# Optimization experiments

Measured on AMD Instinct MI355X. Metric: run time of the kernel, lower is better.

The kernel has to match this reference:

```python
import jax, jax.numpy as jnp
import numpy as np

QPS = 4           # qubits per split
N_SPLITS = 4
N_LAYERS = 4
NUM_CLASSES = 5
DIM = 16          # 2**QPS statevector dim per split
B = 32768

# PauliZ sign table: zsign[q, idx] = +1 if bit of wire q (wire 0 = MSB) is 0 else -1
_ZSIGN = jnp.asarray(
    1 - 2 * (((np.arange(DIM)[None, :] >> (QPS - 1 - np.arange(QPS)[:, None])) & 1)),
    dtype=jnp.float32)  # [QPS, DIM]


def setup_inputs() -> dict:
    key = jax.random.key(0)
    ks = jax.random.split(key, 8)
    return {
        "x": jax.random.normal(ks[0], (B, N_SPLITS * DIM), jnp.float32),
        "split_weights": jax.random.normal(ks[1], (N_SPLITS, N_LAYERS, QPS, 3), jnp.float32) * 0.1,
        "W1": jax.random.normal(ks[2], (N_SPLITS * QPS, 128), jnp.float32) * 0.1,
        "b1": jnp.zeros((128,), jnp.float32),
        "W2": jax.random.normal(ks[3], (128, 64), jnp.float32) * 0.1,
        "b2": jnp.zeros((64,), jnp.float32),
        "W3": jax.random.normal(ks[4], (64, NUM_CLASSES), jnp.float32) * 0.1,
        "b3": jnp.zeros((NUM_CLASSES,), jnp.float32),
    }


def _apply_1q(state, U, wire):
    """Apply per-split 2x2 unitary U [S,2,2] on `wire` of state [B,S,2,2,2,2]."""
    ax = 2 + wire
    st = jnp.moveaxis(state, ax, -1)
    st = jnp.einsum('sij,bs...j->bs...i', U, st)
    return jnp.moveaxis(st, -1, ax)


def _cnot(state, ctrl, tgt):
    c, t = 2 + ctrl, 2 + tgt
    s0 = jnp.take(state, 0, axis=c)
    s1 = jnp.take(state, 1, axis=c)
    s1 = jnp.flip(s1, axis=t - 1 if t > c else t)
    return jnp.stack([s0, s1], axis=c)


def _quantum_features(x, split_weights):
    b = x.shape[0]
    amps = x.reshape(b, N_SPLITS, DIM)
    # _split_data_symmetrically L2-normalizes each chunk (norm>0 guard)
    norm = jnp.linalg.norm(amps, axis=-1, keepdims=True)
    amps = jnp.where(norm > 0, amps / jnp.where(norm > 0, norm, 1.0), amps)
    state = amps.astype(jnp.complex64).reshape((b, N_SPLITS) + (2,) * QPS)
    for layer in range(N_LAYERS):
        for j in range(QPS):
            hx = split_weights[:, layer, j, 0] * 0.5  # [S]
            hy = split_weights[:, layer, j, 1] * 0.5
            hz = split_weights[:, layer, j, 2] * 0.5
            cx, sx = jnp.cos(hx), jnp.sin(hx)
            cy, sy = jnp.cos(hy), jnp.sin(hy)
            RX = jnp.stack([jnp.stack([cx + 0j, -1j * sx], -1),
                            jnp.stack([-1j * sx, cx + 0j], -1)], -2)
            RY = jnp.stack([jnp.stack([cy + 0j, -sy + 0j], -1),
                            jnp.stack([sy + 0j, cy + 0j], -1)], -2)
            ez = jnp.exp(-1j * hz)
            zero = jnp.zeros_like(ez)
            RZ = jnp.stack([jnp.stack([ez, zero], -1),
                            jnp.stack([zero, jnp.conj(ez)], -1)], -2)
            # applied order RX then RY then RZ => U = RZ @ RY @ RX
            U = jnp.einsum('sij,sjk,skl->sil', RZ, RY, RX)
            state = _apply_1q(state, U, j)
        for j in range(QPS):
            state = _cnot(state, j, (j + 1) % QPS)
    probs = (state.real ** 2 + state.imag ** 2).reshape(b, N_SPLITS, DIM)
    exps = jnp.einsum('bsd,qd->bsq', probs, _ZSIGN)  # <PauliZ_q> per split
    return exps.reshape(b, N_SPLITS * QPS)


def reference(x, split_weights, W1, b1, W2, b2, W3, b3):
    feats = _quantum_features(x, split_weights)
    # aggregation MLP (Dropout is identity in eval mode)
    h = jax.nn.relu(feats @ W1 + b1)
    h = jax.nn.relu(h @ W2 + b2)
    return h @ W3 + b3
```

## Files before the change

kernel.cpp:

```cpp
#include <hip/hip_runtime.h>

#define NSPLIT  4
#define NLAYERS 4
#define QPS     4
#define DIM     16
#define NCLS    5
#define BLK     256
#define RROWS   32

#define U_SS      520
#define FE_STRIDE 17
#define H1_STRIDE 33
#define H2_STRIDE 68

struct c32 { float x, y; };
__device__ __forceinline__ c32 cmul(c32 a, c32 b) { return c32{a.x*b.x - a.y*b.y, a.x*b.y + a.y*b.x}; }
__device__ __forceinline__ c32 cadd(c32 a, c32 b) { return c32{a.x + b.x, a.y + b.y}; }

__global__ void build_unitary_kernel(const float* __restrict__ w,
                                     float* __restrict__ Ur,
                                     float* __restrict__ Ui)
{
    __shared__ float gU[NSPLIT][NLAYERS * QPS][8];

    const int t = threadIdx.x;

    {
        const int s = t >> 4, g = t & 15;
        const float* wp = w + (s * (NLAYERS * QPS) + g) * 3;
        const float hx = 0.5f * wp[0], hy = 0.5f * wp[1], hz = 0.5f * wp[2];
        float sx, cx, sy, cy, sz, cz;
        __sincosf(hx, &sx, &cx);
        __sincosf(hy, &sy, &cy);
        __sincosf(hz, &sz, &cz);
        const c32 X00{cx, 0.f}, X01{0.f, -sx}, X11{cx, 0.f};
        const c32 Y00{cy, 0.f}, Y01{-sy, 0.f}, Y10{sy, 0.f}, Y11{cy, 0.f};
        const c32 Z00{cz, -sz}, Z11{cz, sz};
        const c32 M00 = cadd(cmul(Y00, X00), cmul(Y01, X01));
        const c32 M01 = cadd(cmul(Y00, X01), cmul(Y01, X11));
        const c32 M10 = cadd(cmul(Y10, X00), cmul(Y11, X01));
        const c32 M11 = cadd(cmul(Y10, X01), cmul(Y11, X11));
        const c32 U00 = cmul(Z00, M00), U01 = cmul(Z00, M01);
        const c32 U10 = cmul(Z11, M10), U11 = cmul(Z11, M11);
        float* gp = gU[s][g];
        gp[0] = U00.x; gp[1] = U00.y; gp[2] = U01.x; gp[3] = U01.y;
        gp[4] = U10.x; gp[5] = U10.y; gp[6] = U11.x; gp[7] = U11.y;
    }
    __syncthreads();

    const int s = t >> 4, col = t & 15;
    float str[DIM], sti[DIM];
    #pragma unroll
    for (int d = 0; d < DIM; ++d) { str[d] = (d == col) ? 1.0f : 0.0f; sti[d] = 0.0f; }

    #pragma unroll
    for (int l = 0; l < NLAYERS; ++l) {
        #pragma unroll
        for (int j = 0; j < QPS; ++j) {
            const float* gp = gU[s][l * QPS + j];
            const float4 u0 = *(const float4*)gp;
            const float4 u1 = *(const float4*)(gp + 4);
            const int p = 8 >> j;
            #pragma unroll
            for (int i0 = 0; i0 < DIM; ++i0) {
                if (i0 & p) continue;
                const int i1 = i0 | p;
                const float ar = str[i0], ai = sti[i0];
                const float br = str[i1], bi = sti[i1];
                str[i0] = u0.x*ar - u0.y*ai + u0.z*br - u0.w*bi;
                sti[i0] = u0.x*ai + u0.y*ar + u0.z*bi + u0.w*br;
                str[i1] = u1.x*ar - u1.y*ai + u1.z*br - u1.w*bi;
                sti[i1] = u1.x*ai + u1.y*ar + u1.z*bi + u1.w*br;
            }
        }
        #pragma unroll
        for (int j = 0; j < QPS; ++j) {
            const int pc = 8 >> j, pt = 8 >> ((j + 1) & 3);
            #pragma unroll
            for (int i = 0; i < DIM; ++i) {
                if ((i & pc) && !(i & pt)) {
                    const int i1 = i | pt;
                    float tr = str[i]; str[i] = str[i1]; str[i1] = tr;
                    float ti = sti[i]; sti[i] = sti[i1]; sti[i1] = ti;
                }
            }
        }
    }

    #pragma unroll
    for (int d = 0; d < DIM; ++d) {
        Ur[(s * DIM + d) * DIM + col] = str[d];
        Ui[(s * DIM + d) * DIM + col] = sti[d];
    }
}

__global__ __launch_bounds__(BLK) void qcnn_main_kernel(
    const float* __restrict__ x,
    const float* __restrict__ Ug,
    const float* __restrict__ W1, const float* __restrict__ b1,
    const float* __restrict__ W2, const float* __restrict__ b2,
    const float* __restrict__ W3, const float* __restrict__ b3,
    float* __restrict__ out, int B)
{
    __shared__ __align__(16) float sU[NSPLIT * U_SS];
    __shared__ __align__(16) float sW1[128 * 16];
    __shared__ __align__(16) float sW2[128 * 64];
    __shared__ __align__(16) float sFe[RROWS * FE_STRIDE];
    __shared__ __align__(16) float sH1[128 * H1_STRIDE];
    __shared__ __align__(16) float sH2[RROWS * H2_STRIDE];
    __shared__ float sb1[128], sb2[64], sW3b[64 * NCLS], sb3[NCLS];

    const int t = threadIdx.x;
    const int row0 = blockIdx.x * RROWS;

    {
        const float* Urg = Ug;
        const float* Uig = Ug + 1024;
        for (int i = t; i < 1024; i += BLK) {
            const int s = i >> 8, d = (i >> 4) & 15, c = i & 15;
            const int wd = s * U_SS + d * 32 + 2 * c;
            sU[wd] = Urg[i]; sU[wd + 1] = Uig[i];
        }
        for (int i = t; i < 2048; i += BLK) {
            const int k1 = i >> 4, f = i & 15;
            sW1[i] = W1[f * 128 + k1];
        }
        for (int i = t; i < 2048; i += BLK)
            ((float4*)sW2)[i] = ((const float4*)W2)[i];
        if (t < 128) sb1[t] = b1[t];
        if (t < 64)  sb2[t] = b2[t];
        for (int i = t; i < 64 * NCLS; i += BLK) sW3b[i] = W3[i];
        if (t < NCLS) sb3[t] = b3[t];
    }
    __syncthreads();

    {
        const int u = t >> 1, dh = t & 1;
        const int r = u >> 2, s = u & 3;
        int row = row0 + r; if (row >= B) row = B - 1;

        float v[16];
        const float4* xp = (const float4*)(x + (size_t)row * 64 + s * 16);
        const float4 a0 = xp[0], a1 = xp[1], a2 = xp[2], a3 = xp[3];
        v[0]=a0.x;  v[1]=a0.y;  v[2]=a0.z;  v[3]=a0.w;
        v[4]=a1.x;  v[5]=a1.y;  v[6]=a1.z;  v[7]=a1.w;
        v[8]=a2.x;  v[9]=a2.y;  v[10]=a2.z; v[11]=a2.w;
        v[12]=a3.x; v[13]=a3.y; v[14]=a3.z; v[15]=a3.w;

        float n2 = 0.f;
        #pragma unroll
        for (int c = 0; c < 16; ++c) n2 += v[c] * v[c];
        const float inv2 = (n2 > 0.f) ? (1.0f / n2) : 1.0f;

        float e0 = 0.f, e1 = 0.f, e2 = 0.f, e3 = 0.f;
        const float* ub = sU + s * U_SS + dh * (8 * 32);
        #pragma unroll
        for (int i = 0; i < 8; ++i) {
            const int d = dh * 8 + i;
            const float4* up = (const float4*)(ub + i * 32);
            float yr = 0.f, yi = 0.f;
            #pragma unroll
            for (int cp = 0; cp < 8; ++cp) {
                const float4 uu = up[cp];
                yr += uu.x * v[2*cp] + uu.z * v[2*cp + 1];
                yi += uu.y * v[2*cp] + uu.w * v[2*cp + 1];
            }
            const float p = (yr * yr + yi * yi) * inv2;
            e0 += (d & 8) ? -p : p;
            e1 += (d & 4) ? -p : p;
            e2 += (d & 2) ? -p : p;
            e3 += (d & 1) ? -p : p;
        }
        e0 += __shfl_xor(e0, 1);
        e1 += __shfl_xor(e1, 1);
        e2 += __shfl_xor(e2, 1);
        e3 += __shfl_xor(e3, 1);
        if (dh == 0) {
            float* fp = sFe + r * FE_STRIDE + s * 4;
            fp[0] = e0; fp[1] = e1; fp[2] = e2; fp[3] = e3;
        }
    }
    __syncthreads();

    {
        const int r = t & 31, k1g = t >> 5;
        float fv[16];
        #pragma unroll
        for (int f = 0; f < 16; ++f) fv[f] = sFe[r * FE_STRIDE + f];
        #pragma unroll
        for (int kk = 0; kk < 16; ++kk) {
            const int k1 = k1g * 16 + kk;
            const float4* wp = (const float4*)(sW1 + k1 * 16);
            const float4 w0 = wp[0], w1 = wp[1], w2 = wp[2], w3 = wp[3];
            float a = sb1[k1]
                + w0.x*fv[0]  + w0.y*fv[1]  + w0.z*fv[2]  + w0.w*fv[3]
                + w1.x*fv[4]  + w1.y*fv[5]  + w1.z*fv[6]  + w1.w*fv[7]
                + w2.x*fv[8]  + w2.y*fv[9]  + w2.z*fv[10] + w2.w*fv[11]
                + w3.x*fv[12] + w3.y*fv[13] + w3.z*fv[14] + w3.w*fv[15];
            sH1[k1 * H1_STRIDE + r] = fmaxf(a, 0.f);
        }
    }
    __syncthreads();

    {
        const int oct = t & 7, r = t >> 3;
        float acc[8];
        #pragma unroll
        for (int j = 0; j < 8; ++j) acc[j] = sb2[oct * 8 + j];
        const float*  h1p = sH1 + r;
        const float4* w2p = ((const float4*)sW2) + oct * 2;
        #pragma unroll 4
        for (int k1 = 0; k1 < 128; ++k1) {
            const float h = h1p[k1 * H1_STRIDE];
            const float4 wa = w2p[k1 * 16];
            const float4 wb = w2p[k1 * 16 + 1];
            acc[0] += h * wa.x; acc[1] += h * wa.y; acc[2] += h * wa.z; acc[3] += h * wa.w;
            acc[4] += h * wb.x; acc[5] += h * wb.y; acc[6] += h * wb.z; acc[7] += h * wb.w;
        }
        float4 o0, o1;
        o0.x = fmaxf(acc[0], 0.f); o0.y = fmaxf(acc[1], 0.f);
        o0.z = fmaxf(acc[2], 0.f); o0.w = fmaxf(acc[3], 0.f);
        o1.x = fmaxf(acc[4], 0.f); o1.y = fmaxf(acc[5], 0.f);
        o1.z = fmaxf(acc[6], 0.f); o1.w = fmaxf(acc[7], 0.f);
        float4* hp = (float4*)(sH2 + r * H2_STRIDE + oct * 8);
        hp[0] = o0; hp[1] = o1;
    }
    __syncthreads();

    if (t < RROWS * NCLS) {
        const int r = t / NCLS, j = t - r * NCLS;
        float acc = sb3[j];
        const float4* hp = (const float4*)(sH2 + r * H2_STRIDE);
        #pragma unroll
        for (int q = 0; q < 16; ++q) {
            const float4 h = hp[q];
            acc += h.x * sW3b[(4*q + 0) * NCLS + j]
                 + h.y * sW3b[(4*q + 1) * NCLS + j]
                 + h.z * sW3b[(4*q + 2) * NCLS + j]
                 + h.w * sW3b[(4*q + 3) * NCLS + j];
        }
        const int row = row0 + r;
        if (row < B) out[(size_t)row * NCLS + j] = acc;
    }
}

extern "C" void kernel_launch(void* const* d_in, const int* in_sizes, int n_in,
                              void* d_out, int out_size, void* d_ws, size_t ws_size,
                              hipStream_t stream)
{
    (void)n_in; (void)out_size; (void)ws_size;
    const float* x  = (const float*)d_in[0];
    const float* sw = (const float*)d_in[1];
    const float* W1 = (const float*)d_in[2];
    const float* b1 = (const float*)d_in[3];
    const float* W2 = (const float*)d_in[4];
    const float* b2 = (const float*)d_in[5];
    const float* W3 = (const float*)d_in[6];
    const float* b3 = (const float*)d_in[7];
    float* out = (float*)d_out;

    float* Ur = (float*)d_ws;
    float* Ui = Ur + 1024;

    const int B = in_sizes[0] / (NSPLIT * DIM);

    hipLaunchKernelGGL(build_unitary_kernel, dim3(1), dim3(64), 0, stream, sw, Ur, Ui);

    const int grid = (B + RROWS - 1) / RROWS;
    hipLaunchKernelGGL(qcnn_main_kernel, dim3(grid), dim3(BLK), 0, stream,
                       x, (const float*)d_ws, W1, b1, W2, b2, W3, b3, out, B);
}
```

Before: 39.40 us.

## Fuse unitary construction into main kernel and transpose H1 layout for vector loads

The separate single-block unitary-building kernel is removed. Each block now recomputes the 16x16 split unitaries in its first 64 threads while the remaining 192 threads load the MLP weights into shared memory, which eliminates one launch and the workspace round trip. The H1 activation buffer is switched to row-major per sample so layer 2 can read four hidden values per float4 load. The cost is redundant unitary computation in every block, which delays the start of the main work by a serial gate chain.

```diff
diff --git a/kernel.cpp b/kernel.cpp
--- a/kernel.cpp
+++ b/kernel.cpp
@@ -10,22 +10,34 @@
 
 #define U_SS      520
 #define FE_STRIDE 17
-#define H1_STRIDE 33
+#define H1_STRIDE 132
 #define H2_STRIDE 68
 
 struct c32 { float x, y; };
 __device__ __forceinline__ c32 cmul(c32 a, c32 b) { return c32{a.x*b.x - a.y*b.y, a.x*b.y + a.y*b.x}; }
 __device__ __forceinline__ c32 cadd(c32 a, c32 b) { return c32{a.x + b.x, a.y + b.y}; }
 
-__global__ void build_unitary_kernel(const float* __restrict__ w,
-                                     float* __restrict__ Ur,
-                                     float* __restrict__ Ui)
+__global__ __launch_bounds__(BLK) void qcnn_fused_kernel(
+    const float* __restrict__ x,  const float* __restrict__ w,
+    const float* __restrict__ W1, const float* __restrict__ b1,
+    const float* __restrict__ W2, const float* __restrict__ b2,
+    const float* __restrict__ W3, const float* __restrict__ b3,
+    float* __restrict__ out, int B)
 {
-    __shared__ float gU[NSPLIT][NLAYERS * QPS][8];
+    __shared__ __align__(16) float sU[NSPLIT * U_SS];
+    __shared__ __align__(16) float sW1[128 * 16];
+    __shared__ __align__(16) float sW2[128 * 64];
+    __shared__ __align__(16) float sFe[RROWS * FE_STRIDE];
+    __shared__ __align__(16) float sH1[RROWS * H1_STRIDE];
+    __shared__ __align__(16) float sH2[RROWS * H2_STRIDE];
+    __shared__ float sb1[128], sb2[64], sW3b[64 * NCLS], sb3[NCLS];
+
+    float* gUf = sFe;
 
     const int t = threadIdx.x;
-
-    {
+    const int row0 = blockIdx.x * RROWS;
+
+    if (t < 64) {
         const int s = t >> 4, g = t & 15;
         const float* wp = w + (s * (NLAYERS * QPS) + g) * 3;
         const float hx = 0.5f * wp[0], hy = 0.5f * wp[1], hz = 0.5f * wp[2];
@@ -42,95 +54,69 @@
         const c32 M11 = cadd(cmul(Y10, X01), cmul(Y11, X11));
         const c32 U00 = cmul(Z00, M00), U01 = cmul(Z00, M01);
         const c32 U10 = cmul(Z11, M10), U11 = cmul(Z11, M11);
-        float* gp = gU[s][g];
+        float* gp = gUf + s * 128 + g * 8;
         gp[0] = U00.x; gp[1] = U00.y; gp[2] = U01.x; gp[3] = U01.y;
         gp[4] = U10.x; gp[5] = U10.y; gp[6] = U11.x; gp[7] = U11.y;
-    }
-    __syncthreads();
-
-    const int s = t >> 4, col = t & 15;
-    float str[DIM], sti[DIM];
-    #pragma unroll
-    for (int d = 0; d < DIM; ++d) { str[d] = (d == col) ? 1.0f : 0.0f; sti[d] = 0.0f; }
-
-    #pragma unroll
-    for (int l = 0; l < NLAYERS; ++l) {
-        #pragma unroll
-        for (int j = 0; j < QPS; ++j) {
-            const float* gp = gU[s][l * QPS + j];
-            const float4 u0 = *(const float4*)gp;
-            const float4 u1 = *(const float4*)(gp + 4);
-            const int p = 8 >> j;
+    } else {
+        for (int i = t - 64; i < 2048; i += 192)
+            ((float4*)sW2)[i] = ((const float4*)W2)[i];
+    }
+    __syncthreads();
+
+    if (t < 64) {
+        const int s = t >> 4, col = t & 15;
+        float str[DIM], sti[DIM];
+        #pragma unroll
+        for (int d = 0; d < DIM; ++d) { str[d] = (d == col) ? 1.0f : 0.0f; sti[d] = 0.0f; }
+
+        #pragma unroll
+        for (int l = 0; l < NLAYERS; ++l) {
             #pragma unroll
-            for (int i0 = 0; i0 < DIM; ++i0) {
-                if (i0 & p) continue;
-                const int i1 = i0 | p;
-                const float ar = str[i0], ai = sti[i0];
-                const float br = str[i1], bi = sti[i1];
-                str[i0] = u0.x*ar - u0.y*ai + u0.z*br - u0.w*bi;
-                sti[i0] = u0.x*ai + u0.y*ar + u0.z*bi + u0.w*br;
-                str[i1] = u1.x*ar - u1.y*ai + u1.z*br - u1.w*bi;
-                sti[i1] = u1.x*ai + u1.y*ar + u1.z*bi + u1.w*br;
-            }
-        }
-        #pragma unroll
-        for (int j = 0; j < QPS; ++j) {
-            const int pc = 8 >> j, pt = 8 >> ((j + 1) & 3);
+            for (int j = 0; j < QPS; ++j) {
+                const float* gp = gUf + s * 128 + (l * QPS + j) * 8;
+                const float4 u0 = *(const float4*)gp;
+                const float4 u1 = *(const float4*)(gp + 4);
+                const int p = 8 >> j;
+                #pragma unroll
+                for (int i0 = 0; i0 < DIM; ++i0) {
+                    if (i0 & p) continue;
+                    const int i1 = i0 | p;
+                    const float ar = str[i0], ai = sti[i0];
+                    const float br = str[i1], bi = sti[i1];
+                    str[i0] = u0.x*ar - u0.y*ai + u0.z*br - u0.w*bi;
+                    sti[i0] = u0.x*ai + u0.y*ar + u0.z*bi + u0.w*br;
+                    str[i1] = u1.x*ar - u1.y*ai + u1.z*br - u1.w*bi;
+                    sti[i1] = u1.x*ai + u1.y*ar + u1.z*bi + u1.w*br;
+                }
+            }
             #pragma unroll
-            for (int i = 0; i < DIM; ++i) {
-                if ((i & pc) && !(i & pt)) {
-                    const int i1 = i | pt;
-                    float tr = str[i]; str[i] = str[i1]; str[i1] = tr;
-                    float ti = sti[i]; sti[i] = sti[i1]; sti[i1] = ti;
+            for (int j = 0; j < QPS; ++j) {
+                const int pc = 8 >> j, pt = 8 >> ((j + 1) & 3);
+                #pragma unroll
+                for (int i = 0; i < DIM; ++i) {
+                    if ((i & pc) && !(i & pt)) {
+                        const int i1 = i | pt;
+                        float tr = str[i]; str[i] = str[i1]; str[i1] = tr;
+                        float ti = sti[i]; sti[i] = sti[i1]; sti[i1] = ti;
+                    }
                 }
             }
         }
-    }
-
-    #pragma unroll
-    for (int d = 0; d < DIM; ++d) {
-        Ur[(s * DIM + d) * DIM + col] = str[d];
-        Ui[(s * DIM + d) * DIM + col] = sti[d];
-    }
-}
-
-__global__ __launch_bounds__(BLK) void qcnn_main_kernel(
-    const float* __restrict__ x,
-    const float* __restrict__ Ug,
-    const float* __restrict__ W1, const float* __restrict__ b1,
-    const float* __restrict__ W2, const float* __restrict__ b2,
-    const float* __restrict__ W3, const float* __restrict__ b3,
-    float* __restrict__ out, int B)
-{
-    __shared__ __align__(16) float sU[NSPLIT * U_SS];
-    __shared__ __align__(16) float sW1[128 * 16];
-    __shared__ __align__(16) float sW2[128 * 64];
-    __shared__ __align__(16) float sFe[RROWS * FE_STRIDE];
-    __shared__ __align__(16) float sH1[128 * H1_STRIDE];
-    __shared__ __align__(16) float sH2[RROWS * H2_STRIDE];
-    __shared__ float sb1[128], sb2[64], sW3b[64 * NCLS], sb3[NCLS];
-
-    const int t = threadIdx.x;
-    const int row0 = blockIdx.x * RROWS;
-
-    {
-        const float* Urg = Ug;
-        const float* Uig = Ug + 1024;
-        for (int i = t; i < 1024; i += BLK) {
-            const int s = i >> 8, d = (i >> 4) & 15, c = i & 15;
-            const int wd = s * U_SS + d * 32 + 2 * c;
-            sU[wd] = Urg[i]; sU[wd + 1] = Uig[i];
-        }
-        for (int i = t; i < 2048; i += BLK) {
+        #pragma unroll
+        for (int d = 0; d < DIM; ++d) {
+            float2* up = (float2*)(sU + s * U_SS + d * 32 + 2 * col);
+            *up = float2{str[d], sti[d]};
+        }
+    } else {
+        const int tt = t - 64;
+        for (int i = tt; i < 2048; i += 192) {
             const int k1 = i >> 4, f = i & 15;
             sW1[i] = W1[f * 128 + k1];
         }
-        for (int i = t; i < 2048; i += BLK)
-            ((float4*)sW2)[i] = ((const float4*)W2)[i];
-        if (t < 128) sb1[t] = b1[t];
-        if (t < 64)  sb2[t] = b2[t];
-        for (int i = t; i < 64 * NCLS; i += BLK) sW3b[i] = W3[i];
-        if (t < NCLS) sb3[t] = b3[t];
+        for (int i = tt; i < 128;      i += 192) sb1[i] = b1[i];
+        for (int i = tt; i < 64;       i += 192) sb2[i] = b2[i];
+        for (int i = tt; i < 64 * NCLS; i += 192) sW3b[i] = W3[i];
+        for (int i = tt; i < NCLS;     i += 192) sb3[i] = b3[i];
     }
     __syncthreads();
 
@@ -187,6 +173,7 @@
         float fv[16];
         #pragma unroll
         for (int f = 0; f < 16; ++f) fv[f] = sFe[r * FE_STRIDE + f];
+        float res[16];
         #pragma unroll
         for (int kk = 0; kk < 16; ++kk) {
             const int k1 = k1g * 16 + kk;
@@ -197,8 +184,12 @@
                 + w1.x*fv[4]  + w1.y*fv[5]  + w1.z*fv[6]  + w1.w*fv[7]
                 + w2.x*fv[8]  + w2.y*fv[9]  + w2.z*fv[10] + w2.w*fv[11]
                 + w3.x*fv[12] + w3.y*fv[13] + w3.z*fv[14] + w3.w*fv[15];
-            sH1[k1 * H1_STRIDE + r] = fmaxf(a, 0.f);
-        }
+            res[kk] = fmaxf(a, 0.f);
+        }
+        float4* dst = (float4*)(sH1 + r * H1_STRIDE + k1g * 16);
+        #pragma unroll
+        for (int q = 0; q < 4; ++q)
+            dst[q] = float4{res[4*q], res[4*q+1], res[4*q+2], res[4*q+3]};
     }
     __syncthreads();
 
@@ -207,15 +198,31 @@
         float acc[8];
         #pragma unroll
         for (int j = 0; j < 8; ++j) acc[j] = sb2[oct * 8 + j];
-        const float*  h1p = sH1 + r;
+        const float4* h4  = (const float4*)(sH1 + r * H1_STRIDE);
         const float4* w2p = ((const float4*)sW2) + oct * 2;
         #pragma unroll 4
-        for (int k1 = 0; k1 < 128; ++k1) {
-            const float h = h1p[k1 * H1_STRIDE];
-            const float4 wa = w2p[k1 * 16];
-            const float4 wb = w2p[k1 * 16 + 1];
-            acc[0] += h * wa.x; acc[1] += h * wa.y; acc[2] += h * wa.z; acc[3] += h * wa.w;
-            acc[4] += h * wb.x; acc[5] += h * wb.y; acc[6] += h * wb.z; acc[7] += h * wb.w;
+        for (int k4 = 0; k4 < 32; ++k4) {
+            const float4 h = h4[k4];
+            {
+                const float4 wa = w2p[(4*k4+0)*16], wb = w2p[(4*k4+0)*16 + 1];
+                acc[0] += h.x*wa.x; acc[1] += h.x*wa.y; acc[2] += h.x*wa.z; acc[3] += h.x*wa.w;
+                acc[4] += h.x*wb.x; acc[5] += h.x*wb.y; acc[6] += h.x*wb.z; acc[7] += h.x*wb.w;
+            }
+            {
+                const float4 wa = w2p[(4*k4+1)*16], wb = w2p[(4*k4+1)*16 + 1];
+                acc[0] += h.y*wa.x; acc[1] += h.y*wa.y; acc[2] += h.y*wa.z; acc[3] += h.y*wa.w;
+                acc[4] += h.y*wb.x; acc[5] += h.y*wb.y; acc[6] += h.y*wb.z; acc[7] += h.y*wb.w;
+            }
+            {
+                const float4 wa = w2p[(4*k4+2)*16], wb = w2p[(4*k4+2)*16 + 1];
+                acc[0] += h.z*wa.x; acc[1] += h.z*wa.y; acc[2] += h.z*wa.z; acc[3] += h.z*wa.w;
+                acc[4] += h.z*wb.x; acc[5] += h.z*wb.y; acc[6] += h.z*wb.z; acc[7] += h.z*wb.w;
+            }
+            {
+                const float4 wa = w2p[(4*k4+3)*16], wb = w2p[(4*k4+3)*16 + 1];
+                acc[0] += h.w*wa.x; acc[1] += h.w*wa.y; acc[2] += h.w*wa.z; acc[3] += h.w*wa.w;
+                acc[4] += h.w*wb.x; acc[5] += h.w*wb.y; acc[6] += h.w*wb.z; acc[7] += h.w*wb.w;
+            }
         }
         float4 o0, o1;
         o0.x = fmaxf(acc[0], 0.f); o0.y = fmaxf(acc[1], 0.f);
@@ -248,7 +255,7 @@
                               void* d_out, int out_size, void* d_ws, size_t ws_size,
                               hipStream_t stream)
 {
-    (void)n_in; (void)out_size; (void)ws_size;
+    (void)n_in; (void)out_size; (void)d_ws; (void)ws_size;
     const float* x  = (const float*)d_in[0];
     const float* sw = (const float*)d_in[1];
     const float* W1 = (const float*)d_in[2];
@@ -259,14 +266,8 @@
     const float* b3 = (const float*)d_in[7];
     float* out = (float*)d_out;
 
-    float* Ur = (float*)d_ws;
-    float* Ui = Ur + 1024;
-
     const int B = in_sizes[0] / (NSPLIT * DIM);
-
-    hipLaunchKernelGGL(build_unitary_kernel, dim3(1), dim3(64), 0, stream, sw, Ur, Ui);
-
     const int grid = (B + RROWS - 1) / RROWS;
-    hipLaunchKernelGGL(qcnn_main_kernel, dim3(grid), dim3(BLK), 0, stream,
-                       x, (const float*)d_ws, W1, b1, W2, b2, W3, b3, out, B);
+    hipLaunchKernelGGL(qcnn_fused_kernel, dim3(grid), dim3(BLK), 0, stream,
+                       x, sw, W1, b1, W2, b2, W3, b3, out, B);
 }
```

Result: slower. 42.14 us (+6.9%).

## Make each wave own eight rows to drop block barriers after setup

Applied to the files above, without the earlier changes.

Reassigns work so each 64-lane wave handles eight batch rows end to end: features, layer-1, layer-2 and layer-3 all read only that wave's own shared-memory rows. This removes the four __syncthreads between stages. The final layer now reduces through shuffles instead of a separate sH2 buffer. It also swizzles the sW1 layout, pads the feature and hidden strides for float4 access, and sets launch_bounds to 2 blocks, at the cost of more redundant W1 reads per wave and added register pressure.

```diff
diff --git a/kernel.cpp b/kernel.cpp
--- a/kernel.cpp
+++ b/kernel.cpp
@@ -9,9 +9,8 @@
 #define RROWS   32
 
 #define U_SS      520
-#define FE_STRIDE 17
-#define H1_STRIDE 33
-#define H2_STRIDE 68
+#define FE_STRIDE 20
+#define H1_STRIDE 132
 
 struct c32 { float x, y; };
 __device__ __forceinline__ c32 cmul(c32 a, c32 b) { return c32{a.x*b.x - a.y*b.y, a.x*b.y + a.y*b.x}; }
@@ -94,7 +93,7 @@
     }
 }
 
-__global__ __launch_bounds__(BLK) void qcnn_main_kernel(
+__global__ __launch_bounds__(BLK, 2) void qcnn_main_kernel(
     const float* __restrict__ x,
     const float* __restrict__ Ug,
     const float* __restrict__ W1, const float* __restrict__ b1,
@@ -103,14 +102,14 @@
     float* __restrict__ out, int B)
 {
     __shared__ __align__(16) float sU[NSPLIT * U_SS];
-    __shared__ __align__(16) float sW1[128 * 16];
+    __shared__ __align__(16) float sW1[128 * 16 + 32];
     __shared__ __align__(16) float sW2[128 * 64];
     __shared__ __align__(16) float sFe[RROWS * FE_STRIDE];
-    __shared__ __align__(16) float sH1[128 * H1_STRIDE];
-    __shared__ __align__(16) float sH2[RROWS * H2_STRIDE];
-    __shared__ float sb1[128], sb2[64], sW3b[64 * NCLS], sb3[NCLS];
+    __shared__ __align__(16) float sH1[RROWS * H1_STRIDE];
+    __shared__ float sb1[128], sb2[64], sW3b[64 * NCLS], sb3[8];
 
     const int t = threadIdx.x;
+    const int w = t >> 6, lane = t & 63;
     const int row0 = blockIdx.x * RROWS;
 
     {
@@ -123,7 +122,7 @@
         }
         for (int i = t; i < 2048; i += BLK) {
             const int k1 = i >> 4, f = i & 15;
-            sW1[i] = W1[f * 128 + k1];
+            sW1[k1 * 16 + ((k1 >> 4) & 7) * 4 + f] = W1[f * 128 + k1];
         }
         for (int i = t; i < 2048; i += BLK)
             ((float4*)sW2)[i] = ((const float4*)W2)[i];
@@ -135,9 +134,8 @@
     __syncthreads();
 
     {
-        const int u = t >> 1, dh = t & 1;
-        const int r = u >> 2, s = u & 3;
-        int row = row0 + r; if (row >= B) row = B - 1;
+        const int dh = lane & 1, s = (lane >> 1) & 3, rl = lane >> 3;
+        int row = row0 + w * 8 + rl; if (row >= B) row = B - 1;
 
         float v[16];
         const float4* xp = (const float4*)(x + (size_t)row * 64 + s * 16);
@@ -176,71 +174,91 @@
         e2 += __shfl_xor(e2, 1);
         e3 += __shfl_xor(e3, 1);
         if (dh == 0) {
-            float* fp = sFe + r * FE_STRIDE + s * 4;
-            fp[0] = e0; fp[1] = e1; fp[2] = e2; fp[3] = e3;
-        }
-    }
-    __syncthreads();
-
-    {
-        const int r = t & 31, k1g = t >> 5;
-        float fv[16];
-        #pragma unroll
-        for (int f = 0; f < 16; ++f) fv[f] = sFe[r * FE_STRIDE + f];
+            float4* fp = (float4*)(sFe + (w * 8 + rl) * FE_STRIDE + s * 4);
+            *fp = float4{e0, e1, e2, e3};
+        }
+    }
+
+    {
+        const int g = lane & 7, rl = lane >> 3;
+        const float4* fp = (const float4*)(sFe + (w * 8 + rl) * FE_STRIDE);
+        const float4 f0 = fp[0], f1 = fp[1], f2 = fp[2], f3 = fp[3];
+        float res[16];
         #pragma unroll
         for (int kk = 0; kk < 16; ++kk) {
-            const int k1 = k1g * 16 + kk;
-            const float4* wp = (const float4*)(sW1 + k1 * 16);
+            const int k1 = g * 16 + kk;
+            const float4* wp = (const float4*)(sW1 + k1 * 16 + g * 4);
             const float4 w0 = wp[0], w1 = wp[1], w2 = wp[2], w3 = wp[3];
             float a = sb1[k1]
-                + w0.x*fv[0]  + w0.y*fv[1]  + w0.z*fv[2]  + w0.w*fv[3]
-                + w1.x*fv[4]  + w1.y*fv[5]  + w1.z*fv[6]  + w1.w*fv[7]
-                + w2.x*fv[8]  + w2.y*fv[9]  + w2.z*fv[10] + w2.w*fv[11]
-                + w3.x*fv[12] + w3.y*fv[13] + w3.z*fv[14] + w3.w*fv[15];
-            sH1[k1 * H1_STRIDE + r] = fmaxf(a, 0.f);
-        }
-    }
-    __syncthreads();
-
-    {
-        const int oct = t & 7, r = t >> 3;
-        float acc[8];
+                + w0.x*f0.x + w0.y*f0.y + w0.z*f0.z + w0.w*f0.w
+                + w1.x*f1.x + w1.y*f1.y + w1.z*f1.z + w1.w*f1.w
+                + w2.x*f2.x + w2.y*f2.y + w2.z*f2.z + w2.w*f2.w
+                + w3.x*f3.x + w3.y*f3.y + w3.z*f3.z + w3.w*f3.w;
+            res[kk] = fmaxf(a, 0.f);
+        }
+        float4* dst = (float4*)(sH1 + (w * 8 + rl) * H1_STRIDE + g * 16);
+        #pragma unroll
+        for (int q = 0; q < 4; ++q)
+            dst[q] = float4{res[4*q], res[4*q+1], res[4*q+2], res[4*q+3]};
+    }
+
+    float acc[8];
+    {
+        const int oct = lane & 7, rl = lane >> 3;
         #pragma unroll
         for (int j = 0; j < 8; ++j) acc[j] = sb2[oct * 8 + j];
-        const float*  h1p = sH1 + r;
+        const float4* h4  = (const float4*)(sH1 + (w * 8 + rl) * H1_STRIDE);
         const float4* w2p = ((const float4*)sW2) + oct * 2;
         #pragma unroll 4
-        for (int k1 = 0; k1 < 128; ++k1) {
-            const float h = h1p[k1 * H1_STRIDE];
-            const float4 wa = w2p[k1 * 16];
-            const float4 wb = w2p[k1 * 16 + 1];
-            acc[0] += h * wa.x; acc[1] += h * wa.y; acc[2] += h * wa.z; acc[3] += h * wa.w;
-            acc[4] += h * wb.x; acc[5] += h * wb.y; acc[6] += h * wb.z; acc[7] += h * wb.w;
-        }
-        float4 o0, o1;
-        o0.x = fmaxf(acc[0], 0.f); o0.y = fmaxf(acc[1], 0.f);
-        o0.z = fmaxf(acc[2], 0.f); o0.w = fmaxf(acc[3], 0.f);
-        o1.x = fmaxf(acc[4], 0.f); o1.y = fmaxf(acc[5], 0.f);
-        o1.z = fmaxf(acc[6], 0.f); o1.w = fmaxf(acc[7], 0.f);
-        float4* hp = (float4*)(sH2 + r * H2_STRIDE + oct * 8);
-        hp[0] = o0; hp[1] = o1;
-    }
-    __syncthreads();
-
-    if (t < RROWS * NCLS) {
-        const int r = t / NCLS, j = t - r * NCLS;
-        float acc = sb3[j];
-        const float4* hp = (const float4*)(sH2 + r * H2_STRIDE);
-        #pragma unroll
-        for (int q = 0; q < 16; ++q) {
-            const float4 h = hp[q];
-            acc += h.x * sW3b[(4*q + 0) * NCLS + j]
-                 + h.y * sW3b[(4*q + 1) * NCLS + j]
-                 + h.z * sW3b[(4*q + 2) * NCLS + j]
-                 + h.w * sW3b[(4*q + 3) * NCLS + j];
-        }
-        const int row = row0 + r;
-        if (row < B) out[(size_t)row * NCLS + j] = acc;
+        for (int k4 = 0; k4 < 32; ++k4) {
+            const float4 h = h4[k4];
+            {
+                const float4 wa = w2p[(4*k4+0)*16], wb = w2p[(4*k4+0)*16 + 1];
+                acc[0] += h.x*wa.x; acc[1] += h.x*wa.y; acc[2] += h.x*wa.z; acc[3] += h.x*wa.w;
+                acc[4] += h.x*wb.x; acc[5] += h.x*wb.y; acc[6] += h.x*wb.z; acc[7] += h.x*wb.w;
+            }
+            {
+                const float4 wa = w2p[(4*k4+1)*16], wb = w2p[(4*k4+1)*16 + 1];
+                acc[0] += h.y*wa.x; acc[1] += h.y*wa.y; acc[2] += h.y*wa.z; acc[3] += h.y*wa.w;
+                acc[4] += h.y*wb.x; acc[5] += h.y*wb.y; acc[6] += h.y*wb.z; acc[7] += h.y*wb.w;
+            }
+            {
+                const float4 wa = w2p[(4*k4+2)*16], wb = w2p[(4*k4+2)*16 + 1];
+                acc[0] += h.z*wa.x; acc[1] += h.z*wa.y; acc[2] += h.z*wa.z; acc[3] += h.z*wa.w;
+                acc[4] += h.z*wb.x; acc[5] += h.z*wb.y; acc[6] += h.z*wb.z; acc[7] += h.z*wb.w;
+            }
+            {
+                const float4 wa = w2p[(4*k4+3)*16], wb = w2p[(4*k4+3)*16 + 1];
+                acc[0] += h.w*wa.x; acc[1] += h.w*wa.y; acc[2] += h.w*wa.z; acc[3] += h.w*wa.w;
+                acc[4] += h.w*wb.x; acc[5] += h.w*wb.y; acc[6] += h.w*wb.z; acc[7] += h.w*wb.w;
+            }
+        }
+    }
+
+    {
+        const int oct = lane & 7, rl = lane >> 3;
+        float o0 = 0.f, o1 = 0.f, o2 = 0.f, o3 = 0.f, o4 = 0.f;
+        #pragma unroll
+        for (int i = 0; i < 8; ++i) {
+            const float h = fmaxf(acc[i], 0.f);
+            const float* wr = sW3b + (oct * 8 + i) * NCLS;
+            o0 += h * wr[0]; o1 += h * wr[1]; o2 += h * wr[2];
+            o3 += h * wr[3]; o4 += h * wr[4];
+        }
+        #pragma unroll
+        for (int m = 1; m <= 4; m <<= 1) {
+            o0 += __shfl_xor(o0, m);
+            o1 += __shfl_xor(o1, m);
+            o2 += __shfl_xor(o2, m);
+            o3 += __shfl_xor(o3, m);
+            o4 += __shfl_xor(o4, m);
+        }
+        const int row = row0 + w * 8 + rl;
+        if (oct < NCLS && row < B) {
+            const float val = (oct == 0) ? o0 : (oct == 1) ? o1 :
+                              (oct == 2) ? o2 : (oct == 3) ? o3 : o4;
+            out[(size_t)row * NCLS + oct] = val + sb3[oct];
+        }
     }
 }
 
```

New measurement: 39.76 us. Within noise of the previous version (+0.9%).
